# Kernel tuning notes

Measured on AMD Instinct MI355X. Metric: run time of the kernel, lower is better.

Reference implementation:

```python
import jax, jax.numpy as jnp
import numpy as np

N_NODES = 10000


def _add_self_loops(edge_index, n):
    loops = jnp.arange(n, dtype=edge_index.dtype)
    row = jnp.concatenate([edge_index[0], loops])
    col = jnp.concatenate([edge_index[1], loops])
    return row, col


def _gcn_norm(row, col, n):
    # symmetric normalization: deg^-1/2[row] * deg^-1/2[col], deg counted on col
    deg = jax.ops.segment_sum(jnp.ones_like(col, dtype=jnp.float32), col, num_segments=n)
    dis = jnp.where(deg > 0, jax.lax.rsqrt(jnp.maximum(deg, 1.0)), 0.0)
    return dis[row] * dis[col]


def _gcn_conv(x, W, b, row, col, norm, n):
    h = x @ W                      # [N, out]
    m = h[row] * norm[:, None]     # [E+N, out] gathered, normalized messages
    out = jax.ops.segment_sum(m, col, num_segments=n)
    return out + b


def setup_inputs() -> dict:
    key = jax.random.key(0)
    ks = jax.random.split(key, 10)
    N, E, Cin, Cout = N_NODES, 160000, 256, 512
    x = jax.random.normal(ks[0], (N, Cin), dtype=jnp.float32)
    edge_index = jax.random.randint(ks[1], (2, E), 0, N, dtype=jnp.int64)
    s = 1.0 / np.sqrt(Cin)
    s2 = 1.0 / np.sqrt(Cout)
    return {
        "x": x,
        "edge_index": edge_index,
        "W1": jax.random.normal(ks[2], (Cin, Cout), dtype=jnp.float32) * s,
        "b1": jnp.zeros((Cout,), dtype=jnp.float32),
        "W2": jax.random.normal(ks[3], (Cout, Cout), dtype=jnp.float32) * s2,
        "b2": jnp.zeros((Cout,), dtype=jnp.float32),
        "W3": jax.random.normal(ks[4], (Cout, Cout), dtype=jnp.float32) * s2,
        "b3": jnp.zeros((Cout,), dtype=jnp.float32),
        "W4": jax.random.normal(ks[5], (Cout, Cout), dtype=jnp.float32) * s2,
        "b4": jnp.zeros((Cout,), dtype=jnp.float32),
    }


def reference(x, edge_index, W1, b1, W2, b2, W3, b3, W4, b4):
    n = x.shape[0]
    row, col = _add_self_loops(edge_index, n)
    norm = _gcn_norm(row, col, n)
    h = jax.nn.relu(_gcn_conv(x, W1, b1, row, col, norm, n))
    h = jax.nn.relu(_gcn_conv(h, W2, b2, row, col, norm, n))
    h = jax.nn.relu(_gcn_conv(h, W3, b3, row, col, norm, n))
    h = _gcn_conv(h, W4, b4, row, col, norm, n)
    return h.reshape(-1, 5, h.shape[-1])  # [N/5, 5, 512]
```

## Files before the change

kernel.cpp:

```cpp
#include <hip/hip_runtime.h>
#include <hip/hip_bf16.h>

#define N_NODES 10000
#define N_EDGES 160000

typedef __hip_bfloat16 bf16;
typedef unsigned short u16;
typedef float f32x4 __attribute__((ext_vector_type(4)));
typedef short s16x8 __attribute__((ext_vector_type(8)));
typedef unsigned short us8 __attribute__((ext_vector_type(8)));
typedef unsigned short us4 __attribute__((ext_vector_type(4)));

static __device__ __forceinline__ float b2f(u16 u) {
    unsigned v = (unsigned)u << 16;
    return __uint_as_float(v);
}
static __device__ __forceinline__ u16 f2b(float f) {
    bf16 b = __float2bfloat16(f);
    return *reinterpret_cast<u16*>(&b);
}

#define GLDS(gp, lp)                                                         \
    __builtin_amdgcn_global_load_lds(                                        \
        (const __attribute__((address_space(1))) void*)(const void*)(gp),    \
        (__attribute__((address_space(3))) void*)(lp), 16, 0, 0)


__global__ void k_prep(const int* __restrict__ ei, const float* __restrict__ x,
                       u16* __restrict__ xb,
                       int* __restrict__ row, int* __restrict__ col,
                       int* __restrict__ deg) {
    int t = blockIdx.x * 256 + threadIdx.x;
    float4 v = *(const float4*)(x + (size_t)t * 4);
    us4 st;
    st[0] = f2b(v.x); st[1] = f2b(v.y); st[2] = f2b(v.z); st[3] = f2b(v.w);
    *(us4*)(xb + (size_t)t * 4) = st;

    if (t < N_EDGES) {
        bool is64 = true;
#pragma unroll
        for (int k = 0; k < 8; ++k) is64 = is64 && (ei[2 * k + 1] == 0);
        int r, c;
        if (is64) {
            r = ei[2 * t];
            c = ei[2 * (N_EDGES + t)];
        } else {
            r = ei[t];
            c = ei[N_EDGES + t];
        }
        row[t] = r;
        col[t] = c;
        atomicAdd(&deg[c], 1);
    }
}

__global__ void k_scan_all(const int* __restrict__ deg, float* __restrict__ dis,
                           int* __restrict__ off, int* __restrict__ cur) {
    __shared__ int sd[N_NODES];
    __shared__ int sums[256];
    int t = threadIdx.x;
    for (int i = t; i < N_NODES; i += 256) {
        int d = deg[i];
        sd[i] = d;
        dis[i] = rsqrtf((float)d + 1.0f);
    }
    __syncthreads();
    const int seg = (N_NODES + 255) >> 8;
    int lo = t * seg, hi = lo + seg;
    if (lo > N_NODES) lo = N_NODES;
    if (hi > N_NODES) hi = N_NODES;
    int s = 0;
    for (int i = lo; i < hi; ++i) s += sd[i];
    sums[t] = s;
    __syncthreads();
    for (int d = 1; d < 256; d <<= 1) {
        int v = (t >= d) ? sums[t - d] : 0;
        __syncthreads();
        sums[t] += v;
        __syncthreads();
    }
    int run = sums[t] - s;
    for (int i = lo; i < hi; ++i) {
        off[i] = run;
        cur[i] = run;
        run += sd[i];
    }
    if (t == 255) off[N_NODES] = sums[255];
}


__global__ void k_fill_t(const int* __restrict__ row, const int* __restrict__ col,
                         const float* __restrict__ dis, int* cur,
                         int* __restrict__ crow, float* __restrict__ cnorm,
                         const float* __restrict__ W1, const float* __restrict__ W2,
                         const float* __restrict__ W3, const float* __restrict__ W4,
                         u16* __restrict__ T1, u16* __restrict__ T2,
                         u16* __restrict__ T3, u16* __restrict__ T4) {
    __shared__ u16 tile[32][33];
    if (blockIdx.x < 625) {
        int e = blockIdx.x * 256 + threadIdx.x;
        if (e < N_EDGES) {
            int r = row[e], c = col[e];
            int p = atomicAdd(&cur[c], 1);
            crow[p] = r;
            cnorm[p] = dis[r] * dis[c];
        }
        return;
    }
    int b = blockIdx.x - 625;
    int z = b >> 8;
    int rem = b & 255;
    int by = rem >> 4, bx = rem & 15;
    const float* W = (z == 0) ? W1 : (z == 1) ? W2 : (z == 2) ? W3 : W4;
    u16* WT        = (z == 0) ? T1 : (z == 1) ? T2 : (z == 2) ? T3 : T4;
    int K = (z == 0) ? 256 : 512;
    int k0 = by * 32;
    if (k0 >= K) return;
    int n0 = bx * 32;
    int tx = threadIdx.x & 31, ty = threadIdx.x >> 5;
    for (int i = 0; i < 32; i += 8)
        tile[ty + i][tx] = f2b(W[(size_t)(k0 + ty + i) * 512 + n0 + tx]);
    __syncthreads();
    for (int i = 0; i < 32; i += 8)
        WT[(size_t)(n0 + ty + i) * K + k0 + tx] = tile[tx][ty + i];
}


template <int CE> struct VecT;
template <> struct VecT<4> { typedef us4 T; };
template <> struct VecT<8> { typedef us8 T; };

template <int CE>
__global__ void k_agg(const u16* __restrict__ in, u16* __restrict__ out,
                      const int* __restrict__ off, const int* __restrict__ crow,
                      const float* __restrict__ cnorm, const float* __restrict__ dis) {
    typedef typename VecT<CE>::T VT;
    const int C = CE * 64;
    int node = blockIdx.x * 4 + (threadIdx.x >> 6);
    int lane = threadIdx.x & 63;
    int c = lane * CE;

    float d = dis[node];
    VT sv = *(const VT*)(in + (size_t)node * C + c);
    float a0[CE], a1[CE], a2[CE], a3[CE];
#pragma unroll
    for (int j = 0; j < CE; ++j) {
        a0[j] = b2f(sv[j]) * d * d;
        a1[j] = 0.f; a2[j] = 0.f; a3[j] = 0.f;
    }

    int b = off[node], e = off[node + 1];
    int i = b;
    for (; i + 7 < e; i += 8) {
        int r[8]; float nn[8]; VT v[8];
#pragma unroll
        for (int q = 0; q < 8; ++q) { r[q] = crow[i + q]; nn[q] = cnorm[i + q]; }
#pragma unroll
        for (int q = 0; q < 8; ++q) v[q] = *(const VT*)(in + (size_t)r[q] * C + c);
#pragma unroll
        for (int j = 0; j < CE; ++j) {
            a0[j] = fmaf(b2f(v[0][j]), nn[0], a0[j]);
            a1[j] = fmaf(b2f(v[1][j]), nn[1], a1[j]);
            a2[j] = fmaf(b2f(v[2][j]), nn[2], a2[j]);
            a3[j] = fmaf(b2f(v[3][j]), nn[3], a3[j]);
        }
#pragma unroll
        for (int j = 0; j < CE; ++j) {
            a0[j] = fmaf(b2f(v[4][j]), nn[4], a0[j]);
            a1[j] = fmaf(b2f(v[5][j]), nn[5], a1[j]);
            a2[j] = fmaf(b2f(v[6][j]), nn[6], a2[j]);
            a3[j] = fmaf(b2f(v[7][j]), nn[7], a3[j]);
        }
    }
    for (; i + 3 < e; i += 4) {
        int r0 = crow[i], r1 = crow[i + 1], r2 = crow[i + 2], r3 = crow[i + 3];
        float n0 = cnorm[i], n1 = cnorm[i + 1], n2 = cnorm[i + 2], n3 = cnorm[i + 3];
        VT v0 = *(const VT*)(in + (size_t)r0 * C + c);
        VT v1 = *(const VT*)(in + (size_t)r1 * C + c);
        VT v2 = *(const VT*)(in + (size_t)r2 * C + c);
        VT v3 = *(const VT*)(in + (size_t)r3 * C + c);
#pragma unroll
        for (int j = 0; j < CE; ++j) {
            a0[j] = fmaf(b2f(v0[j]), n0, a0[j]);
            a1[j] = fmaf(b2f(v1[j]), n1, a1[j]);
            a2[j] = fmaf(b2f(v2[j]), n2, a2[j]);
            a3[j] = fmaf(b2f(v3[j]), n3, a3[j]);
        }
    }
    for (; i < e; ++i) {
        int r0 = crow[i];
        float n0 = cnorm[i];
        VT v0 = *(const VT*)(in + (size_t)r0 * C + c);
#pragma unroll
        for (int j = 0; j < CE; ++j) a0[j] = fmaf(b2f(v0[j]), n0, a0[j]);
    }
    VT st;
#pragma unroll
    for (int j = 0; j < CE; ++j) st[j] = f2b((a0[j] + a1[j]) + (a2[j] + a3[j]));
    *(VT*)(out + (size_t)node * C + c) = st;
}


static __device__ __forceinline__ void st_out(float* out, size_t idx, float v) { out[idx] = v; }
static __device__ __forceinline__ void st_out(u16* out, size_t idx, float v) { out[idx] = f2b(v); }

static __device__ __forceinline__ void gemm_stage(
        u16 (*Asb)[64][32], u16 (*Bsb)[128][32],
        const u16* const G[6], const int isA[6],
        const int P[6], const int R[6], int kk) {
#pragma unroll
    for (int q = 0; q < 6; ++q) {
        if (isA[q]) GLDS(G[q] + kk, &Asb[P[q]][R[q]][0]);
        else        GLDS(G[q] + kk, &Bsb[P[q]][R[q]][0]);
    }
}

static __device__ __forceinline__ void gemm_compute(
        const u16 (*Asb)[64][32], const u16 (*Bsb)[128][32],
        int wm, int wn, int l15, int kq, f32x4 acc[2][4]) {
#pragma unroll
    for (int p = 0; p < 2; ++p) {
        s16x8 a[2], bb[4];
#pragma unroll
        for (int mi = 0; mi < 2; ++mi)
            a[mi] = *(const s16x8*)&Asb[p][wm * 32 + mi * 16 + l15][kq * 8];
#pragma unroll
        for (int ni = 0; ni < 4; ++ni)
            bb[ni] = *(const s16x8*)&Bsb[p][wn * 64 + ni * 16 + l15][kq * 8];
#pragma unroll
        for (int mi = 0; mi < 2; ++mi)
#pragma unroll
            for (int ni = 0; ni < 4; ++ni)
                acc[mi][ni] = __builtin_amdgcn_mfma_f32_16x16x32_bf16(
                    a[mi], bb[ni], acc[mi][ni], 0, 0, 0);
    }
}

template <typename OT>
__global__ __launch_bounds__(256, 3) void k_gemm(
        const u16* __restrict__ A, const u16* __restrict__ BT,
        const float* __restrict__ bias, OT* __restrict__ out,
        int M, int K, int NO, int relu) {
    __shared__ u16 As[2][2][64][32];
    __shared__ u16 Bs[2][2][128][32];

    int tid = threadIdx.x;
    int w = tid >> 6;
    int lane = tid & 63;
    int wm = w >> 1, wn = w & 1;
    int n0 = blockIdx.x * 128;
    int m0 = blockIdx.y * 64;
    int l15 = lane & 15;
    int kq = lane >> 4;

    int srow = lane >> 2;
    int skc = (lane & 3) * 8;

    const u16* G[6];
    int isA[6], P[6], R[6];
#pragma unroll
    for (int q = 0; q < 6; ++q) {
        int ch = w * 6 + q;
        if (ch < 8) {
            isA[q] = 1;
            P[q] = ch >> 2;
            R[q] = (ch & 3) * 16;
            int ar = m0 + R[q] + srow;
            if (ar > M - 1) ar = M - 1;
            G[q] = A + (size_t)ar * K + P[q] * 32 + skc;
        } else {
            int cb = ch - 8;
            isA[q] = 0;
            P[q] = cb >> 3;
            R[q] = (cb & 7) * 16;
            int br = n0 + R[q] + srow;
            G[q] = BT + (size_t)br * K + P[q] * 32 + skc;
        }
    }

    f32x4 acc[2][4];
#pragma unroll
    for (int mi = 0; mi < 2; ++mi)
#pragma unroll
        for (int ni = 0; ni < 4; ++ni) acc[mi][ni] = (f32x4){0.f, 0.f, 0.f, 0.f};

    int NT = K >> 6;
    gemm_stage(As[0], Bs[0], G, isA, P, R, 0);
    __syncthreads();
    for (int t = 0; t < NT; t += 2) {
        gemm_stage(As[1], Bs[1], G, isA, P, R, (t + 1) * 64);
        gemm_compute(As[0], Bs[0], wm, wn, l15, kq, acc);
        __syncthreads();
        if (t + 2 < NT)
            gemm_stage(As[0], Bs[0], G, isA, P, R, (t + 2) * 64);
        gemm_compute(As[1], Bs[1], wm, wn, l15, kq, acc);
        __syncthreads();
    }

    int r0o = (lane >> 4) * 4;
    int cm = m0 + wm * 32;
    int cn = n0 + wn * 64;
    float bv[4];
#pragma unroll
    for (int ni = 0; ni < 4; ++ni) bv[ni] = bias[cn + ni * 16 + l15];
#pragma unroll
    for (int mi = 0; mi < 2; ++mi) {
#pragma unroll
        for (int r = 0; r < 4; ++r) {
            int rowa = cm + mi * 16 + r0o + r;
            if (rowa < M) {
#pragma unroll
                for (int ni = 0; ni < 4; ++ni) {
                    float v = acc[mi][ni][r] + bv[ni];
                    if (relu) v = fmaxf(v, 0.f);
                    st_out(out, (size_t)rowa * NO + cn + ni * 16 + l15, v);
                }
            }
        }
    }
}


extern "C" void kernel_launch(void* const* d_in, const int* in_sizes, int n_in,
                              void* d_out, int out_size, void* d_ws, size_t ws_size,
                              hipStream_t stream) {
    const float* x  = (const float*)d_in[0];
    const int*   ei = (const int*)d_in[1];
    const float* W1 = (const float*)d_in[2];
    const float* b1 = (const float*)d_in[3];
    const float* W2 = (const float*)d_in[4];
    const float* b2 = (const float*)d_in[5];
    const float* W3 = (const float*)d_in[6];
    const float* b3 = (const float*)d_in[7];
    const float* W4 = (const float*)d_in[8];
    const float* b4 = (const float*)d_in[9];

    char* ws = (char*)d_ws;
    size_t o = 0;
    auto alloc = [&](size_t bytes) {
        char* p = ws + o;
        o = (o + bytes + 255) & ~(size_t)255;
        return p;
    };
    int*   row   = (int*)alloc(N_EDGES * 4);
    int*   col   = (int*)alloc(N_EDGES * 4);
    int*   deg   = (int*)alloc(N_NODES * 4);
    float* dis   = (float*)alloc(N_NODES * 4);
    int*   off   = (int*)alloc((N_NODES + 1) * 4);
    int*   cur   = (int*)alloc(N_NODES * 4);
    int*   crow  = (int*)alloc(N_EDGES * 4);
    float* cnorm = (float*)alloc(N_EDGES * 4);
    u16*   WT1   = (u16*)alloc((size_t)512 * 256 * 2);
    u16*   WT2   = (u16*)alloc((size_t)512 * 512 * 2);
    u16*   WT3   = (u16*)alloc((size_t)512 * 512 * 2);
    u16*   WT4   = (u16*)alloc((size_t)512 * 512 * 2);
    u16*   xb    = (u16*)alloc((size_t)N_NODES * 256 * 2);
    u16*   s     = (u16*)alloc((size_t)N_NODES * 512 * 2);
    u16*   h     = (u16*)alloc((size_t)N_NODES * 512 * 2);
    float* outb  = (float*)d_out;

    dim3 b256(256);
    const dim3 gG(4, 157);
    const int  gA = (N_NODES + 3) / 4;
    const int  gP = N_NODES * 256 / 4 / 256;

    hipMemsetAsync(deg, 0, N_NODES * 4, stream);
    k_prep<<<gP, b256, 0, stream>>>(ei, x, xb, row, col, deg);
    k_scan_all<<<1, b256, 0, stream>>>(deg, dis, off, cur);
    k_fill_t<<<625 + 1024, b256, 0, stream>>>(row, col, dis, cur, crow, cnorm,
                                              W1, W2, W3, W4, WT1, WT2, WT3, WT4);

    k_agg<4><<<gA, b256, 0, stream>>>(xb, s, off, crow, cnorm, dis);
    k_gemm<u16><<<gG, b256, 0, stream>>>(s, WT1, b1, h, N_NODES, 256, 512, 1);
    k_agg<8><<<gA, b256, 0, stream>>>(h, s, off, crow, cnorm, dis);
    k_gemm<u16><<<gG, b256, 0, stream>>>(s, WT2, b2, h, N_NODES, 512, 512, 1);
    k_agg<8><<<gA, b256, 0, stream>>>(h, s, off, crow, cnorm, dis);
    k_gemm<u16><<<gG, b256, 0, stream>>>(s, WT3, b3, h, N_NODES, 512, 512, 1);
    k_agg<8><<<gA, b256, 0, stream>>>(h, s, off, crow, cnorm, dis);
    k_gemm<float><<<gG, b256, 0, stream>>>(s, WT4, b4, outb, N_NODES, 512, 512, 0);
}
```

Before: 261.2 us.

## Split aggregation across channel slices with consecutive blocks sharing nodes

The aggregation kernel now assigns each block a 128-channel slice of four nodes, with slice index in the low bits of the block id, so adjacent blocks gather the same neighbour rows. Each lane loads 4 bytes instead of 8 or 16, which raises the block count and parallelism and may improve L2 reuse of gathered rows across slices. In exchange, edge index and norm loads are repeated per slice, and each gather is narrower.

After: 264.1 us. About the same (+1.1%).

```diff
diff --git a/kernel.cpp b/kernel.cpp
--- a/kernel.cpp
+++ b/kernel.cpp
@@ -126,78 +126,71 @@
 }
 
 
-template <int CE> struct VecT;
-template <> struct VecT<4> { typedef us4 T; };
-template <> struct VecT<8> { typedef us8 T; };
-
-template <int CE>
-__global__ void k_agg(const u16* __restrict__ in, u16* __restrict__ out,
-                      const int* __restrict__ off, const int* __restrict__ crow,
-                      const float* __restrict__ cnorm, const float* __restrict__ dis) {
-    typedef typename VecT<CE>::T VT;
-    const int C = CE * 64;
-    int node = blockIdx.x * 4 + (threadIdx.x >> 6);
+template <int C, int LSL>
+__global__ void k_agg_sl(const u16* __restrict__ in, u16* __restrict__ out,
+                         const int* __restrict__ off, const int* __restrict__ crow,
+                         const float* __restrict__ cnorm, const float* __restrict__ dis) {
+    int b = blockIdx.x;
+    int slice = b & ((1 << LSL) - 1);
+    int g = b >> LSL;
+    int node = g * 4 + (threadIdx.x >> 6);
     int lane = threadIdx.x & 63;
-    int c = lane * CE;
-
-    float d = dis[node];
-    VT sv = *(const VT*)(in + (size_t)node * C + c);
-    float a0[CE], a1[CE], a2[CE], a3[CE];
-#pragma unroll
-    for (int j = 0; j < CE; ++j) {
-        a0[j] = b2f(sv[j]) * d * d;
-        a1[j] = 0.f; a2[j] = 0.f; a3[j] = 0.f;
-    }
-
-    int b = off[node], e = off[node + 1];
-    int i = b;
-    for (; i + 7 < e; i += 8) {
-        int r[8]; float nn[8]; VT v[8];
+    const u16* inp = in + (size_t)slice * 128 + lane * 2;
+    u16* outp      = out + (size_t)slice * 128 + lane * 2;
+
+    float dn = dis[node];
+    unsigned sv = *(const unsigned*)(inp + (size_t)node * C);
+    float aa0 = b2f((u16)(sv & 0xffff)) * dn * dn;
+    float aa1 = b2f((u16)(sv >> 16)) * dn * dn;
+    float bb0 = 0.f, bb1 = 0.f, cc0 = 0.f, cc1 = 0.f, dd0 = 0.f, dd1 = 0.f;
+
+    int lo = off[node], hi = off[node + 1];
+    int i = lo;
+    for (; i + 7 < hi; i += 8) {
+        int r[8]; float nn[8]; unsigned v[8];
 #pragma unroll
         for (int q = 0; q < 8; ++q) { r[q] = crow[i + q]; nn[q] = cnorm[i + q]; }
 #pragma unroll
-        for (int q = 0; q < 8; ++q) v[q] = *(const VT*)(in + (size_t)r[q] * C + c);
-#pragma unroll
-        for (int j = 0; j < CE; ++j) {
-            a0[j] = fmaf(b2f(v[0][j]), nn[0], a0[j]);
-            a1[j] = fmaf(b2f(v[1][j]), nn[1], a1[j]);
-            a2[j] = fmaf(b2f(v[2][j]), nn[2], a2[j]);
-            a3[j] = fmaf(b2f(v[3][j]), nn[3], a3[j]);
-        }
-#pragma unroll
-        for (int j = 0; j < CE; ++j) {
-            a0[j] = fmaf(b2f(v[4][j]), nn[4], a0[j]);
-            a1[j] = fmaf(b2f(v[5][j]), nn[5], a1[j]);
-            a2[j] = fmaf(b2f(v[6][j]), nn[6], a2[j]);
-            a3[j] = fmaf(b2f(v[7][j]), nn[7], a3[j]);
-        }
-    }
-    for (; i + 3 < e; i += 4) {
+        for (int q = 0; q < 8; ++q) v[q] = *(const unsigned*)(inp + (size_t)r[q] * C);
+#pragma unroll
+        for (int q = 0; q < 8; q += 4) {
+            aa0 = fmaf(b2f((u16)(v[q] & 0xffff)), nn[q], aa0);
+            aa1 = fmaf(b2f((u16)(v[q] >> 16)), nn[q], aa1);
+            bb0 = fmaf(b2f((u16)(v[q + 1] & 0xffff)), nn[q + 1], bb0);
+            bb1 = fmaf(b2f((u16)(v[q + 1] >> 16)), nn[q + 1], bb1);
+            cc0 = fmaf(b2f((u16)(v[q + 2] & 0xffff)), nn[q + 2], cc0);
+            cc1 = fmaf(b2f((u16)(v[q + 2] >> 16)), nn[q + 2], cc1);
+            dd0 = fmaf(b2f((u16)(v[q + 3] & 0xffff)), nn[q + 3], dd0);
+            dd1 = fmaf(b2f((u16)(v[q + 3] >> 16)), nn[q + 3], dd1);
+        }
+    }
+    for (; i + 3 < hi; i += 4) {
         int r0 = crow[i], r1 = crow[i + 1], r2 = crow[i + 2], r3 = crow[i + 3];
         float n0 = cnorm[i], n1 = cnorm[i + 1], n2 = cnorm[i + 2], n3 = cnorm[i + 3];
-        VT v0 = *(const VT*)(in + (size_t)r0 * C + c);
-        VT v1 = *(const VT*)(in + (size_t)r1 * C + c);
-        VT v2 = *(const VT*)(in + (size_t)r2 * C + c);
-        VT v3 = *(const VT*)(in + (size_t)r3 * C + c);
-#pragma unroll
-        for (int j = 0; j < CE; ++j) {
-            a0[j] = fmaf(b2f(v0[j]), n0, a0[j]);
-            a1[j] = fmaf(b2f(v1[j]), n1, a1[j]);
-            a2[j] = fmaf(b2f(v2[j]), n2, a2[j]);
-            a3[j] = fmaf(b2f(v3[j]), n3, a3[j]);
-        }
-    }
-    for (; i < e; ++i) {
+        unsigned v0 = *(const unsigned*)(inp + (size_t)r0 * C);
+        unsigned v1 = *(const unsigned*)(inp + (size_t)r1 * C);
+        unsigned v2 = *(const unsigned*)(inp + (size_t)r2 * C);
+        unsigned v3 = *(const unsigned*)(inp + (size_t)r3 * C);
+        aa0 = fmaf(b2f((u16)(v0 & 0xffff)), n0, aa0);
+        aa1 = fmaf(b2f((u16)(v0 >> 16)), n0, aa1);
+        bb0 = fmaf(b2f((u16)(v1 & 0xffff)), n1, bb0);
+        bb1 = fmaf(b2f((u16)(v1 >> 16)), n1, bb1);
+        cc0 = fmaf(b2f((u16)(v2 & 0xffff)), n2, cc0);
+        cc1 = fmaf(b2f((u16)(v2 >> 16)), n2, cc1);
+        dd0 = fmaf(b2f((u16)(v3 & 0xffff)), n3, dd0);
+        dd1 = fmaf(b2f((u16)(v3 >> 16)), n3, dd1);
+    }
+    for (; i < hi; ++i) {
         int r0 = crow[i];
         float n0 = cnorm[i];
-        VT v0 = *(const VT*)(in + (size_t)r0 * C + c);
-#pragma unroll
-        for (int j = 0; j < CE; ++j) a0[j] = fmaf(b2f(v0[j]), n0, a0[j]);
-    }
-    VT st;
-#pragma unroll
-    for (int j = 0; j < CE; ++j) st[j] = f2b((a0[j] + a1[j]) + (a2[j] + a3[j]));
-    *(VT*)(out + (size_t)node * C + c) = st;
+        unsigned v0 = *(const unsigned*)(inp + (size_t)r0 * C);
+        aa0 = fmaf(b2f((u16)(v0 & 0xffff)), n0, aa0);
+        aa1 = fmaf(b2f((u16)(v0 >> 16)), n0, aa1);
+    }
+    float e0 = (aa0 + bb0) + (cc0 + dd0);
+    float e1 = (aa1 + bb1) + (cc1 + dd1);
+    unsigned st = (unsigned)f2b(e0) | ((unsigned)f2b(e1) << 16);
+    *(unsigned*)(outp + (size_t)node * C) = st;
 }
 
 
@@ -361,8 +354,9 @@
 
     dim3 b256(256);
     const dim3 gG(4, 157);
-    const int  gA = (N_NODES + 3) / 4;
     const int  gP = N_NODES * 256 / 4 / 256;
+    const int  gA1 = 2500 * 2;
+    const int  gA  = 2500 * 4;
 
     hipMemsetAsync(deg, 0, N_NODES * 4, stream);
     k_prep<<<gP, b256, 0, stream>>>(ei, x, xb, row, col, deg);
@@ -370,12 +364,12 @@
     k_fill_t<<<625 + 1024, b256, 0, stream>>>(row, col, dis, cur, crow, cnorm,
                                               W1, W2, W3, W4, WT1, WT2, WT3, WT4);
 
-    k_agg<4><<<gA, b256, 0, stream>>>(xb, s, off, crow, cnorm, dis);
+    k_agg_sl<256, 1><<<gA1, b256, 0, stream>>>(xb, s, off, crow, cnorm, dis);
     k_gemm<u16><<<gG, b256, 0, stream>>>(s, WT1, b1, h, N_NODES, 256, 512, 1);
-    k_agg<8><<<gA, b256, 0, stream>>>(h, s, off, crow, cnorm, dis);
+    k_agg_sl<512, 2><<<gA, b256, 0, stream>>>(h, s, off, crow, cnorm, dis);
     k_gemm<u16><<<gG, b256, 0, stream>>>(s, WT2, b2, h, N_NODES, 512, 512, 1);
-    k_agg<8><<<gA, b256, 0, stream>>>(h, s, off, crow, cnorm, dis);
+    k_agg_sl<512, 2><<<gA, b256, 0, stream>>>(h, s, off, crow, cnorm, dis);
     k_gemm<u16><<<gG, b256, 0, stream>>>(s, WT3, b3, h, N_NODES, 512, 512, 1);
-    k_agg<8><<<gA, b256, 0, stream>>>(h, s, off, crow, cnorm, dis);
+    k_agg_sl<512, 2><<<gA, b256, 0, stream>>>(h, s, off, crow, cnorm, dis);
     k_gemm<float><<<gG, b256, 0, stream>>>(s, WT4, b4, outb, N_NODES, 512, 512, 0);
 }
```

## Move weight transpose into prep kernel and software-prefetch edge indices in aggregation

Applied to the files above, without the earlier changes.

The bf16 weight transpose/convert blocks move from the CSR fill kernel into the prep kernel, so they run alongside the x conversion and degree counting. The fill kernel then only does the edge scatter. Separately, the aggregation loop now loads the next batch of 8 edge indices and norms while the current batch's gathers are in flight. This hides index-load latency on top of the gathered-row latency, at the cost of more registers per thread and therefore possibly lower occupancy.

After: 262.0 us. No clear change (+0.3%).

```diff
diff --git a/kernel.cpp b/kernel.cpp
--- a/kernel.cpp
+++ b/kernel.cpp
@@ -29,85 +29,38 @@
 __global__ void k_prep(const int* __restrict__ ei, const float* __restrict__ x,
                        u16* __restrict__ xb,
                        int* __restrict__ row, int* __restrict__ col,
-                       int* __restrict__ deg) {
-    int t = blockIdx.x * 256 + threadIdx.x;
-    float4 v = *(const float4*)(x + (size_t)t * 4);
-    us4 st;
-    st[0] = f2b(v.x); st[1] = f2b(v.y); st[2] = f2b(v.z); st[3] = f2b(v.w);
-    *(us4*)(xb + (size_t)t * 4) = st;
-
-    if (t < N_EDGES) {
-        bool is64 = true;
-#pragma unroll
-        for (int k = 0; k < 8; ++k) is64 = is64 && (ei[2 * k + 1] == 0);
-        int r, c;
-        if (is64) {
-            r = ei[2 * t];
-            c = ei[2 * (N_EDGES + t)];
-        } else {
-            r = ei[t];
-            c = ei[N_EDGES + t];
-        }
-        row[t] = r;
-        col[t] = c;
-        atomicAdd(&deg[c], 1);
-    }
-}
-
-__global__ void k_scan_all(const int* __restrict__ deg, float* __restrict__ dis,
-                           int* __restrict__ off, int* __restrict__ cur) {
-    __shared__ int sd[N_NODES];
-    __shared__ int sums[256];
-    int t = threadIdx.x;
-    for (int i = t; i < N_NODES; i += 256) {
-        int d = deg[i];
-        sd[i] = d;
-        dis[i] = rsqrtf((float)d + 1.0f);
-    }
-    __syncthreads();
-    const int seg = (N_NODES + 255) >> 8;
-    int lo = t * seg, hi = lo + seg;
-    if (lo > N_NODES) lo = N_NODES;
-    if (hi > N_NODES) hi = N_NODES;
-    int s = 0;
-    for (int i = lo; i < hi; ++i) s += sd[i];
-    sums[t] = s;
-    __syncthreads();
-    for (int d = 1; d < 256; d <<= 1) {
-        int v = (t >= d) ? sums[t - d] : 0;
-        __syncthreads();
-        sums[t] += v;
-        __syncthreads();
-    }
-    int run = sums[t] - s;
-    for (int i = lo; i < hi; ++i) {
-        off[i] = run;
-        cur[i] = run;
-        run += sd[i];
-    }
-    if (t == 255) off[N_NODES] = sums[255];
-}
-
-
-__global__ void k_fill_t(const int* __restrict__ row, const int* __restrict__ col,
-                         const float* __restrict__ dis, int* cur,
-                         int* __restrict__ crow, float* __restrict__ cnorm,
-                         const float* __restrict__ W1, const float* __restrict__ W2,
-                         const float* __restrict__ W3, const float* __restrict__ W4,
-                         u16* __restrict__ T1, u16* __restrict__ T2,
-                         u16* __restrict__ T3, u16* __restrict__ T4) {
+                       int* __restrict__ deg,
+                       const float* __restrict__ W1, const float* __restrict__ W2,
+                       const float* __restrict__ W3, const float* __restrict__ W4,
+                       u16* __restrict__ T1, u16* __restrict__ T2,
+                       u16* __restrict__ T3, u16* __restrict__ T4) {
     __shared__ u16 tile[32][33];
-    if (blockIdx.x < 625) {
-        int e = blockIdx.x * 256 + threadIdx.x;
-        if (e < N_EDGES) {
-            int r = row[e], c = col[e];
-            int p = atomicAdd(&cur[c], 1);
-            crow[p] = r;
-            cnorm[p] = dis[r] * dis[c];
+    if (blockIdx.x < 2500) {
+        int t = blockIdx.x * 256 + threadIdx.x;
+        float4 v = *(const float4*)(x + (size_t)t * 4);
+        us4 st;
+        st[0] = f2b(v.x); st[1] = f2b(v.y); st[2] = f2b(v.z); st[3] = f2b(v.w);
+        *(us4*)(xb + (size_t)t * 4) = st;
+
+        if (t < N_EDGES) {
+            bool is64 = true;
+#pragma unroll
+            for (int k = 0; k < 8; ++k) is64 = is64 && (ei[2 * k + 1] == 0);
+            int r, c;
+            if (is64) {
+                r = ei[2 * t];
+                c = ei[2 * (N_EDGES + t)];
+            } else {
+                r = ei[t];
+                c = ei[N_EDGES + t];
+            }
+            row[t] = r;
+            col[t] = c;
+            atomicAdd(&deg[c], 1);
         }
         return;
     }
-    int b = blockIdx.x - 625;
+    int b = blockIdx.x - 2500;
     int z = b >> 8;
     int rem = b & 255;
     int by = rem >> 4, bx = rem & 15;
@@ -125,6 +78,53 @@
         WT[(size_t)(n0 + ty + i) * K + k0 + tx] = tile[tx][ty + i];
 }
 
+__global__ void k_scan_all(const int* __restrict__ deg, float* __restrict__ dis,
+                           int* __restrict__ off, int* __restrict__ cur) {
+    __shared__ int sd[N_NODES];
+    __shared__ int sums[256];
+    int t = threadIdx.x;
+    for (int i = t; i < N_NODES; i += 256) {
+        int d = deg[i];
+        sd[i] = d;
+        dis[i] = rsqrtf((float)d + 1.0f);
+    }
+    __syncthreads();
+    const int seg = (N_NODES + 255) >> 8;
+    int lo = t * seg, hi = lo + seg;
+    if (lo > N_NODES) lo = N_NODES;
+    if (hi > N_NODES) hi = N_NODES;
+    int s = 0;
+    for (int i = lo; i < hi; ++i) s += sd[i];
+    sums[t] = s;
+    __syncthreads();
+    for (int d = 1; d < 256; d <<= 1) {
+        int v = (t >= d) ? sums[t - d] : 0;
+        __syncthreads();
+        sums[t] += v;
+        __syncthreads();
+    }
+    int run = sums[t] - s;
+    for (int i = lo; i < hi; ++i) {
+        off[i] = run;
+        cur[i] = run;
+        run += sd[i];
+    }
+    if (t == 255) off[N_NODES] = sums[255];
+}
+
+
+__global__ void k_fill(const int* __restrict__ row, const int* __restrict__ col,
+                       const float* __restrict__ dis, int* cur,
+                       int* __restrict__ crow, float* __restrict__ cnorm) {
+    int e = blockIdx.x * 256 + threadIdx.x;
+    if (e < N_EDGES) {
+        int r = row[e], c = col[e];
+        int p = atomicAdd(&cur[c], 1);
+        crow[p] = r;
+        cnorm[p] = dis[r] * dis[c];
+    }
+}
+
 
 template <int CE> struct VecT;
 template <> struct VecT<4> { typedef us4 T; };
@@ -149,30 +149,56 @@
         a1[j] = 0.f; a2[j] = 0.f; a3[j] = 0.f;
     }
 
-    int b = off[node], e = off[node + 1];
-    int i = b;
-    for (; i + 7 < e; i += 8) {
-        int r[8]; float nn[8]; VT v[8];
-#pragma unroll
-        for (int q = 0; q < 8; ++q) { r[q] = crow[i + q]; nn[q] = cnorm[i + q]; }
-#pragma unroll
-        for (int q = 0; q < 8; ++q) v[q] = *(const VT*)(in + (size_t)r[q] * C + c);
-#pragma unroll
-        for (int j = 0; j < CE; ++j) {
-            a0[j] = fmaf(b2f(v[0][j]), nn[0], a0[j]);
-            a1[j] = fmaf(b2f(v[1][j]), nn[1], a1[j]);
-            a2[j] = fmaf(b2f(v[2][j]), nn[2], a2[j]);
-            a3[j] = fmaf(b2f(v[3][j]), nn[3], a3[j]);
+    int i = off[node], hi = off[node + 1];
+    int rA[8]; float nA[8];
+    if (i + 8 <= hi) {
+#pragma unroll
+        for (int q = 0; q < 8; ++q) { rA[q] = crow[i + q]; nA[q] = cnorm[i + q]; }
+    }
+    while (i + 8 <= hi) {
+        VT v[8];
+#pragma unroll
+        for (int q = 0; q < 8; ++q) v[q] = *(const VT*)(in + (size_t)rA[q] * C + c);
+        int inext = i + 8;
+        if (inext + 8 <= hi) {
+            int rB[8]; float nB[8];
+#pragma unroll
+            for (int q = 0; q < 8; ++q) { rB[q] = crow[inext + q]; nB[q] = cnorm[inext + q]; }
+#pragma unroll
+            for (int j = 0; j < CE; ++j) {
+                a0[j] = fmaf(b2f(v[0][j]), nA[0], a0[j]);
+                a1[j] = fmaf(b2f(v[1][j]), nA[1], a1[j]);
+                a2[j] = fmaf(b2f(v[2][j]), nA[2], a2[j]);
+                a3[j] = fmaf(b2f(v[3][j]), nA[3], a3[j]);
+            }
+#pragma unroll
+            for (int j = 0; j < CE; ++j) {
+                a0[j] = fmaf(b2f(v[4][j]), nA[4], a0[j]);
+                a1[j] = fmaf(b2f(v[5][j]), nA[5], a1[j]);
+                a2[j] = fmaf(b2f(v[6][j]), nA[6], a2[j]);
+                a3[j] = fmaf(b2f(v[7][j]), nA[7], a3[j]);
+            }
+#pragma unroll
+            for (int q = 0; q < 8; ++q) { rA[q] = rB[q]; nA[q] = nB[q]; }
+        } else {
+#pragma unroll
+            for (int j = 0; j < CE; ++j) {
+                a0[j] = fmaf(b2f(v[0][j]), nA[0], a0[j]);
+                a1[j] = fmaf(b2f(v[1][j]), nA[1], a1[j]);
+                a2[j] = fmaf(b2f(v[2][j]), nA[2], a2[j]);
+                a3[j] = fmaf(b2f(v[3][j]), nA[3], a3[j]);
+            }
+#pragma unroll
+            for (int j = 0; j < CE; ++j) {
+                a0[j] = fmaf(b2f(v[4][j]), nA[4], a0[j]);
+                a1[j] = fmaf(b2f(v[5][j]), nA[5], a1[j]);
+                a2[j] = fmaf(b2f(v[6][j]), nA[6], a2[j]);
+                a3[j] = fmaf(b2f(v[7][j]), nA[7], a3[j]);
+            }
         }
-#pragma unroll
-        for (int j = 0; j < CE; ++j) {
-            a0[j] = fmaf(b2f(v[4][j]), nn[4], a0[j]);
-            a1[j] = fmaf(b2f(v[5][j]), nn[5], a1[j]);
-            a2[j] = fmaf(b2f(v[6][j]), nn[6], a2[j]);
-            a3[j] = fmaf(b2f(v[7][j]), nn[7], a3[j]);
-        }
-    }
-    for (; i + 3 < e; i += 4) {
+        i = inext;
+    }
+    for (; i + 3 < hi; i += 4) {
         int r0 = crow[i], r1 = crow[i + 1], r2 = crow[i + 2], r3 = crow[i + 3];
         float n0 = cnorm[i], n1 = cnorm[i + 1], n2 = cnorm[i + 2], n3 = cnorm[i + 3];
         VT v0 = *(const VT*)(in + (size_t)r0 * C + c);
@@ -187,7 +213,7 @@
             a3[j] = fmaf(b2f(v3[j]), n3, a3[j]);
         }
     }
-    for (; i < e; ++i) {
+    for (; i < hi; ++i) {
         int r0 = crow[i];
         float n0 = cnorm[i];
         VT v0 = *(const VT*)(in + (size_t)r0 * C + c);
@@ -362,13 +388,12 @@
     dim3 b256(256);
     const dim3 gG(4, 157);
     const int  gA = (N_NODES + 3) / 4;
-    const int  gP = N_NODES * 256 / 4 / 256;
 
     hipMemsetAsync(deg, 0, N_NODES * 4, stream);
-    k_prep<<<gP, b256, 0, stream>>>(ei, x, xb, row, col, deg);
+    k_prep<<<2500 + 1024, b256, 0, stream>>>(ei, x, xb, row, col, deg,
+                                             W1, W2, W3, W4, WT1, WT2, WT3, WT4);
     k_scan_all<<<1, b256, 0, stream>>>(deg, dis, off, cur);
-    k_fill_t<<<625 + 1024, b256, 0, stream>>>(row, col, dis, cur, crow, cnorm,
-                                              W1, W2, W3, W4, WT1, WT2, WT3, WT4);
+    k_fill<<<625, b256, 0, stream>>>(row, col, dis, cur, crow, cnorm);
 
     k_agg<4><<<gA, b256, 0, stream>>>(xb, s, off, crow, cnorm, dis);
     k_gemm<u16><<<gG, b256, 0, stream>>>(s, WT1, b1, h, N_NODES, 256, 512, 1);
```
